# Kernel optimization log

Measured on AMD Instinct MI355X. Metric: run time of the kernel, lower is better.

The kernel has to match this reference:

```python
import jax, jax.numpy as jnp
from jax import lax
import numpy as np

S, B, XD = 2048, 64, 64   # seq_len, batch, x_dim
DX = 128                   # dense_x[-1]
H = 256                    # dim_RNN
DH = 128                   # dense_h_x[-1]
ALPHAS = np.array([0.9, 0.5, 0.1, 0.01], dtype=np.float32)


def setup_inputs() -> dict:
    key = jax.random.key(0)
    ks = jax.random.split(key, 12)
    def lin(k, fan_in, shape):
        return jax.random.normal(k, shape, jnp.float32) / np.sqrt(fan_in)
    sigmas = jnp.asarray(-np.log(1.0 / ALPHAS - 1.0), jnp.float32)  # inverse sigmoid
    return {
        "x": jax.random.normal(ks[0], (S, B, XD), jnp.float32),
        "Wx": lin(ks[1], XD, (XD, DX)),   # feature_extractor_x linear
        "bx": jnp.zeros((DX,), jnp.float32),
        "Wih": lin(ks[2], DX, (H, DX)),   # RNN input-hidden
        "bih": jnp.zeros((H,), jnp.float32),
        "Whh": lin(ks[3], H, (H, H)),     # RNN hidden-hidden
        "bhh": jnp.zeros((H,), jnp.float32),
        "Whx": lin(ks[4], H, (H, DH)),    # mlp_h_x linear
        "bhx": jnp.zeros((DH,), jnp.float32),
        "Wout": lin(ks[5], DH, (DH, XD)), # gen_out
        "bout": jnp.zeros((XD,), jnp.float32),
        "sigmas": sigmas,
    }


def reference(x, Wx, bx, Wih, bih, Whh, bhh, Whx, bhx, Wout, bout, sigmas):
    # alphas_per_unit: sigmoid(sigmas) tiled to dim_RNN
    alphas = jnp.tile(jax.nn.sigmoid(sigmas), H // sigmas.shape[0])  # [H]
    # feature extractor over all timesteps (teacher forcing, mix_ratio=0)
    feat = jnp.tanh(x @ Wx + bx)  # [S, B, DX]
    h0 = jnp.zeros((x.shape[1], H), x.dtype)

    def step(h, f_t):
        # emit y_t from previous hidden state: gen_out(tanh(mlp_h_x(h)))
        y_t = jnp.tanh(h @ Whx + bhx) @ Wout + bout        # [B, XD]
        # single-step Elman RNN cell
        h_new = jnp.tanh(f_t @ Wih.T + bih + h @ Whh.T + bhh)
        # leaky integration blend per unit
        h_next = (1.0 - alphas) * h + alphas * h_new
        return h_next, y_t

    _, y = lax.scan(step, h0, feat)  # y: [S, B, XD]
    return y
```

## Files before the change

### kernel.cpp

```cpp
#include <hip/hip_runtime.h>
#include <math.h>

#define SS 2048
#define BB 64
#define XDIM 64
#define DXF 128
#define HH 256
#define DHH 128
#define CHUNK 16
#define NW (SS / CHUNK)

typedef float v2f __attribute__((ext_vector_type(2)));

__device__ __forceinline__ float ftanh(float x) {
    float e = __expf(2.0f * x);
    return 1.0f - 2.0f / (e + 1.0f);
}

template <int CTRL>
__device__ __forceinline__ float dpp_mov_f(float x) {
    return __int_as_float(__builtin_amdgcn_update_dpp(
        0, __float_as_int(x), CTRL, 0xF, 0xF, true));
}

__global__ __launch_bounds__(256) void k1_featu(
    const float* __restrict__ x, const float* __restrict__ Wx,
    const float* __restrict__ bx, const float* __restrict__ Wih,
    const float* __restrict__ bih, const float* __restrict__ bhh,
    float* __restrict__ u)
{
    __shared__ float xs[64][XDIM];
    __shared__ float fs[64][DXF];
    const int tid = threadIdx.x;
    const size_t row0 = (size_t)blockIdx.x * 64;

    for (int v = tid; v < 64 * XDIM; v += 256) {
        int r = v >> 6, m = v & 63;
        xs[r][m] = x[(row0 + r) * XDIM + m];
    }
    __syncthreads();

    {
        const int cq = tid & 31;
        const int ru = tid >> 5;
        v2f aA[2][4], aB[2][4];
        #pragma unroll
        for (int g = 0; g < 2; ++g)
            #pragma unroll
            for (int i = 0; i < 4; ++i) { aA[g][i] = (v2f)0.f; aB[g][i] = (v2f)0.f; }

        #pragma unroll
        for (int kc = 0; kc < 4; ++kc) {
            v2f wA[16], wB[16];
            #pragma unroll
            for (int k = 0; k < 16; ++k) {
                const float* wp = Wx + (kc * 16 + k) * DXF + cq;
                wA[k] = (v2f){wp[0],  wp[32]};
                wB[k] = (v2f){wp[64], wp[96]};
            }
            #pragma unroll
            for (int g = 0; g < 2; ++g) {
                const int rb = 8 * ru + 4 * g;
                #pragma unroll
                for (int k4 = 0; k4 < 4; ++k4) {
                    float4 xv[4];
                    #pragma unroll
                    for (int i = 0; i < 4; ++i)
                        xv[i] = *(const float4*)&xs[rb + i][kc * 16 + 4 * k4];
                    #pragma unroll
                    for (int i = 0; i < 4; ++i) {
                        #pragma unroll
                        for (int e = 0; e < 4; ++e) {
                            const float xe = (e == 0) ? xv[i].x : (e == 1) ? xv[i].y
                                           : (e == 2) ? xv[i].z : xv[i].w;
                            const v2f xb = (v2f){xe, xe};
                            aA[g][i] += wA[4 * k4 + e] * xb;
                            aB[g][i] += wB[4 * k4 + e] * xb;
                        }
                    }
                }
            }
        }
        const float b0 = bx[cq], b1 = bx[cq + 32], b2 = bx[cq + 64], b3 = bx[cq + 96];
        #pragma unroll
        for (int g = 0; g < 2; ++g)
            #pragma unroll
            for (int i = 0; i < 4; ++i) {
                const int r = 8 * ru + 4 * g + i;
                fs[r][cq]      = ftanh(aA[g][i].x + b0);
                fs[r][cq + 32] = ftanh(aA[g][i].y + b1);
                fs[r][cq + 64] = ftanh(aB[g][i].x + b2);
                fs[r][cq + 96] = ftanh(aB[g][i].y + b3);
            }
    }
    __syncthreads();

    {
        const int q4 = tid & 63;
        const int rq = tid >> 6;
        v2f aA[4][4], aB[4][4];
        #pragma unroll
        for (int g = 0; g < 4; ++g)
            #pragma unroll
            for (int i = 0; i < 4; ++i) { aA[g][i] = (v2f)0.f; aB[g][i] = (v2f)0.f; }

        #pragma unroll
        for (int kc = 0; kc < 8; ++kc) {
            v2f wA[16], wB[16];
            #pragma unroll
            for (int k4 = 0; k4 < 4; ++k4) {
                const float4 w0 = *(const float4*)(Wih + (size_t)(q4      ) * DXF + kc * 16 + 4 * k4);
                const float4 w1 = *(const float4*)(Wih + (size_t)(q4 +  64) * DXF + kc * 16 + 4 * k4);
                const float4 w2 = *(const float4*)(Wih + (size_t)(q4 + 128) * DXF + kc * 16 + 4 * k4);
                const float4 w3 = *(const float4*)(Wih + (size_t)(q4 + 192) * DXF + kc * 16 + 4 * k4);
                wA[4 * k4 + 0] = (v2f){w0.x, w1.x}; wA[4 * k4 + 1] = (v2f){w0.y, w1.y};
                wA[4 * k4 + 2] = (v2f){w0.z, w1.z}; wA[4 * k4 + 3] = (v2f){w0.w, w1.w};
                wB[4 * k4 + 0] = (v2f){w2.x, w3.x}; wB[4 * k4 + 1] = (v2f){w2.y, w3.y};
                wB[4 * k4 + 2] = (v2f){w2.z, w3.z}; wB[4 * k4 + 3] = (v2f){w2.w, w3.w};
            }
            #pragma unroll
            for (int g = 0; g < 4; ++g) {
                const int rb = 16 * rq + 4 * g;
                #pragma unroll
                for (int k4 = 0; k4 < 4; ++k4) {
                    float4 fv[4];
                    #pragma unroll
                    for (int i = 0; i < 4; ++i)
                        fv[i] = *(const float4*)&fs[rb + i][kc * 16 + 4 * k4];
                    #pragma unroll
                    for (int i = 0; i < 4; ++i) {
                        #pragma unroll
                        for (int e = 0; e < 4; ++e) {
                            const float fe = (e == 0) ? fv[i].x : (e == 1) ? fv[i].y
                                           : (e == 2) ? fv[i].z : fv[i].w;
                            const v2f fb = (v2f){fe, fe};
                            aA[g][i] += wA[4 * k4 + e] * fb;
                            aB[g][i] += wB[4 * k4 + e] * fb;
                        }
                    }
                }
            }
        }
        const float b0 = bih[q4]       + bhh[q4];
        const float b1 = bih[q4 + 64]  + bhh[q4 + 64];
        const float b2 = bih[q4 + 128] + bhh[q4 + 128];
        const float b3 = bih[q4 + 192] + bhh[q4 + 192];
        #pragma unroll
        for (int g = 0; g < 4; ++g)
            #pragma unroll
            for (int i = 0; i < 4; ++i) {
                const size_t row = row0 + 16 * rq + 4 * g + i;
                u[row * HH + q4]       = aA[g][i].x + b0;
                u[row * HH + q4 + 64]  = aA[g][i].y + b1;
                u[row * HH + q4 + 128] = aB[g][i].x + b2;
                u[row * HH + q4 + 192] = aB[g][i].y + b3;
            }
    }
}

__global__ __launch_bounds__(1024)
__attribute__((amdgpu_waves_per_eu(4, 4)))
void k2_rnn(
    const float* __restrict__ u, const float* __restrict__ Whh,
    const float* __restrict__ sigmas, float* __restrict__ hist)
{
    __shared__ float hbuf[2][HH];
    __shared__ float ubuf[2][CHUNK][HH];
    const int tid = threadIdx.x;
    const int b = blockIdx.x;
    const int c  = tid & 15;
    const int rg = tid >> 4;

    v2f w2[4][8];
    #pragma unroll
    for (int r = 0; r < 4; ++r) {
        const float* wrow = Whh + (size_t)(4 * rg + r) * HH + 16 * c;
        #pragma unroll
        for (int j = 0; j < 4; ++j) {
            const float4 wv = *(const float4*)(wrow + 4 * j);
            w2[r][2 * j]     = (v2f){wv.x, wv.y};
            w2[r][2 * j + 1] = (v2f){wv.z, wv.w};
        }
    }
    #pragma unroll
    for (int r = 0; r < 4; r += 2) {
        asm volatile("" : "+v"(w2[r][0]),     "+v"(w2[r][1]),     "+v"(w2[r][2]),     "+v"(w2[r][3]),
                          "+v"(w2[r][4]),     "+v"(w2[r][5]),     "+v"(w2[r][6]),     "+v"(w2[r][7]),
                          "+v"(w2[r + 1][0]), "+v"(w2[r + 1][1]), "+v"(w2[r + 1][2]), "+v"(w2[r + 1][3]),
                          "+v"(w2[r + 1][4]), "+v"(w2[r + 1][5]), "+v"(w2[r + 1][6]), "+v"(w2[r + 1][7]));
    }

    const int pb0 = c & 1;
    const int pb3 = (c >> 3) & 1;
    const int rl = 2 * pb3 + pb0;
    const int myrow = 4 * rg + rl;
    const bool own = ((c & 6) == 0);

    const float alpha = 1.f / (1.f + __expf(-sigmas[myrow & 3]));

    const int wpos = 64 * ((myrow >> 2) & 3) + 4 * (myrow >> 4) + (myrow & 3);

    const int srow = tid >> 6;
    const int col4 = tid & 63;
    const size_t ustride = (size_t)BB * HH;

    if (tid < HH) hbuf[0][tid] = 0.0f;

    {
        const float4 v = *(const float4*)(u + ((size_t)srow * BB + b) * HH + 4 * col4);
        *(float4*)&ubuf[0][srow][4 * col4] = v;
    }

    float* hp = hist + (size_t)b * HH + myrow;
    float hreg = 0.f;

    __syncthreads();

#define K2_BODY(T, S, MBUF, DO_STAGE, NBUF)                                  \
    {                                                                        \
        const int cur = (T) & 1;                                             \
        const float uval = ubuf[MBUF][S][myrow];                             \
        float4 h4[4];                                                        \
        _Pragma("unroll")                                                    \
        for (int j = 0; j < 4; ++j)                                          \
            h4[j] = *(const float4*)&hbuf[cur][64 * j + 4 * c];              \
        v2f acc[4];                                                          \
        _Pragma("unroll")                                                    \
        for (int r = 0; r < 4; ++r) acc[r] = (v2f)0.f;                       \
        _Pragma("unroll")                                                    \
        for (int j = 0; j < 4; ++j) {                                        \
            const v2f hA = (v2f){h4[j].x, h4[j].y};                          \
            const v2f hB = (v2f){h4[j].z, h4[j].w};                          \
            _Pragma("unroll")                                                \
            for (int r = 0; r < 4; ++r) {                                    \
                acc[r] += w2[r][2 * j] * hA;                                 \
                acc[r] += w2[r][2 * j + 1] * hB;                             \
            }                                                                \
        }                                                                    \
        float s_[4];                                                         \
        _Pragma("unroll")                                                    \
        for (int r = 0; r < 4; ++r) s_[r] = acc[r].x + acc[r].y;             \
                   \
        float t1[2];                                                         \
        _Pragma("unroll")                                                    \
        for (int i = 0; i < 2; ++i) {                                        \
            const float g = pb3 ? s_[i] : s_[i + 2];                         \
            const float k = pb3 ? s_[i + 2] : s_[i];                         \
            t1[i] = k + dpp_mov_f<0x128>(g);                                 \
        }                                                                    \
                \
        float sr;                                                            \
        {                                                                    \
            const float g = pb0 ? t1[0] : t1[1];                             \
            const float k = pb0 ? t1[1] : t1[0];                             \
            sr = k + dpp_mov_f<0xB1>(g);                                     \
        }                                                                    \
                            \
        sr += dpp_mov_f<0x4E>(sr);                                           \
                           \
        sr += __int_as_float(__builtin_amdgcn_ds_swizzle(                    \
                  __float_as_int(sr), 0x101F));                              \
        {                                                                    \
            const float sin_ = sr + uval;                                    \
            const float hnew = hreg + alpha * (ftanh(sin_) - hreg);          \
            if (own) {                                                       \
                *hp = hreg;                        \
                hbuf[cur ^ 1][wpos] = hnew;                                  \
            }                                                                \
            hreg = hnew;                                                     \
        }                                                                    \
        hp += ustride;                                                       \
        if (DO_STAGE) {                                                      \
             \
             \
            *(float4*)&ubuf[NBUF][srow][4 * col4] = stv;                     \
        }                                                                    \
                   \
        asm volatile("s_waitcnt lgkmcnt(0)\n\ts_barrier" ::: "memory");      \
    }

    for (int m = 0; m < NW; ++m) {
        const int mbuf = m & 1;
        const int nbuf = mbuf ^ 1;
        const bool more = (m + 1 < NW);
        float4 stv;
        if (more) {
            const size_t t0 = (size_t)(CHUNK * (m + 1));
            stv = *(const float4*)(u + ((t0 + srow) * BB + b) * HH + 4 * col4);
        }
        #pragma unroll 4
        for (int s = 0; s < CHUNK; ++s) {
            const int t = CHUNK * m + s;
            const bool stage = (s == CHUNK - 1) && more;
            K2_BODY(t, s, mbuf, stage, nbuf)
        }
    }
#undef K2_BODY
}

__global__ __launch_bounds__(256) void k3_y(
    const float* __restrict__ hist, const float* __restrict__ Whx,
    const float* __restrict__ bhx, const float* __restrict__ Wout,
    const float* __restrict__ bout, float* __restrict__ y)
{
    __shared__ float hs[32][HH];
    __shared__ float gs[32][DHH];
    const int tid = threadIdx.x;
    const size_t row0 = (size_t)blockIdx.x * 32;

    for (int v = tid; v < 32 * HH; v += 256) {
        int r = v >> 8, i = v & 255;
        hs[r][i] = hist[(row0 + r) * HH + i];
    }
    __syncthreads();

    {
        const int aq = tid & 31;
        const int ru = tid >> 5;
        v2f aA[4], aB[4];
        #pragma unroll
        for (int i = 0; i < 4; ++i) { aA[i] = (v2f)0.f; aB[i] = (v2f)0.f; }

        #pragma unroll
        for (int kc = 0; kc < 16; ++kc) {
            v2f wA[16], wB[16];
            #pragma unroll
            for (int k = 0; k < 16; ++k) {
                const float* wp = Whx + (size_t)(kc * 16 + k) * DHH + aq;
                wA[k] = (v2f){wp[0],  wp[32]};
                wB[k] = (v2f){wp[64], wp[96]};
            }
            #pragma unroll
            for (int k4 = 0; k4 < 4; ++k4) {
                float4 hv[4];
                #pragma unroll
                for (int i = 0; i < 4; ++i)
                    hv[i] = *(const float4*)&hs[4 * ru + i][kc * 16 + 4 * k4];
                #pragma unroll
                for (int i = 0; i < 4; ++i) {
                    #pragma unroll
                    for (int e = 0; e < 4; ++e) {
                        const float he = (e == 0) ? hv[i].x : (e == 1) ? hv[i].y
                                       : (e == 2) ? hv[i].z : hv[i].w;
                        const v2f hb = (v2f){he, he};
                        aA[i] += wA[4 * k4 + e] * hb;
                        aB[i] += wB[4 * k4 + e] * hb;
                    }
                }
            }
        }
        const float b0 = bhx[aq], b1 = bhx[aq + 32], b2 = bhx[aq + 64], b3 = bhx[aq + 96];
        #pragma unroll
        for (int i = 0; i < 4; ++i) {
            const int r = 4 * ru + i;
            gs[r][aq]      = ftanh(aA[i].x + b0);
            gs[r][aq + 32] = ftanh(aA[i].y + b1);
            gs[r][aq + 64] = ftanh(aB[i].x + b2);
            gs[r][aq + 96] = ftanh(aB[i].y + b3);
        }
    }
    __syncthreads();

    {
        const int o2 = tid & 31;
        const int ru = tid >> 5;
        v2f acc[4];
        #pragma unroll
        for (int i = 0; i < 4; ++i) acc[i] = (v2f)0.f;

        #pragma unroll
        for (int kc = 0; kc < 2; ++kc) {
            v2f w[64];
            #pragma unroll
            for (int k = 0; k < 64; ++k) {
                const float* wp = Wout + (size_t)(kc * 64 + k) * XDIM + o2;
                w[k] = (v2f){wp[0], wp[32]};
            }
            #pragma unroll
            for (int k4 = 0; k4 < 16; ++k4) {
                float4 gv[4];
                #pragma unroll
                for (int i = 0; i < 4; ++i)
                    gv[i] = *(const float4*)&gs[4 * ru + i][kc * 64 + 4 * k4];
                #pragma unroll
                for (int i = 0; i < 4; ++i) {
                    #pragma unroll
                    for (int e = 0; e < 4; ++e) {
                        const float ge = (e == 0) ? gv[i].x : (e == 1) ? gv[i].y
                                       : (e == 2) ? gv[i].z : gv[i].w;
                        acc[i] += w[4 * k4 + e] * (v2f){ge, ge};
                    }
                }
            }
        }
        const float b0 = bout[o2], b1 = bout[o2 + 32];
        #pragma unroll
        for (int i = 0; i < 4; ++i) {
            const size_t row = row0 + 4 * ru + i;
            y[row * XDIM + o2]      = acc[i].x + b0;
            y[row * XDIM + o2 + 32] = acc[i].y + b1;
        }
    }
}

extern "C" void kernel_launch(void* const* d_in, const int* in_sizes, int n_in,
                              void* d_out, int out_size, void* d_ws, size_t ws_size,
                              hipStream_t stream) {
    const float* x      = (const float*)d_in[0];
    const float* Wx     = (const float*)d_in[1];
    const float* bx     = (const float*)d_in[2];
    const float* Wih    = (const float*)d_in[3];
    const float* bih    = (const float*)d_in[4];
    const float* Whh    = (const float*)d_in[5];
    const float* bhh    = (const float*)d_in[6];
    const float* Whx    = (const float*)d_in[7];
    const float* bhx    = (const float*)d_in[8];
    const float* Wout   = (const float*)d_in[9];
    const float* bout   = (const float*)d_in[10];
    const float* sigmas = (const float*)d_in[11];
    float* y = (float*)d_out;

    float* u    = (float*)d_ws;
    float* hist = u + (size_t)SS * BB * HH;

    k1_featu<<<(SS * BB) / 64, 256, 0, stream>>>(x, Wx, bx, Wih, bih, bhh, u);
    k2_rnn<<<BB, 1024, 0, stream>>>(u, Whh, sigmas, hist);
    k3_y<<<(SS * BB) / 32, 256, 0, stream>>>(hist, Whx, bhx, Wout, bout, y);
}
```

Baseline: 1.956 ms.

## Halve RNN block to 512 threads with eight Whh rows per thread

The recurrent kernel now launches 512 threads per batch element instead of 1024. Each thread holds eight rows of Whh in registers instead of four, and the cross-lane reduction gains one more DPP butterfly stage. Staging of the u chunk is split into two float4 loads per thread. The aim is to cut per-step barrier and synchronisation cost across fewer waves, at the price of more register pressure and a longer serial FMA chain per step.

Result: faster. 1.804 ms (-7.8%).

```diff
diff --git a/kernel.cpp b/kernel.cpp
--- a/kernel.cpp
+++ b/kernel.cpp
@@ -158,8 +158,7 @@
     }
 }
 
-__global__ __launch_bounds__(1024)
-__attribute__((amdgpu_waves_per_eu(4, 4)))
+__global__ __launch_bounds__(512)
 void k2_rnn(
     const float* __restrict__ u, const float* __restrict__ Whh,
     const float* __restrict__ sigmas, float* __restrict__ hist)
@@ -171,10 +170,10 @@
     const int c  = tid & 15;
     const int rg = tid >> 4;
 
-    v2f w2[4][8];
+    v2f w2[8][8];
     #pragma unroll
-    for (int r = 0; r < 4; ++r) {
-        const float* wrow = Whh + (size_t)(4 * rg + r) * HH + 16 * c;
+    for (int r = 0; r < 8; ++r) {
+        const float* wrow = Whh + (size_t)(8 * rg + r) * HH + 16 * c;
         #pragma unroll
         for (int j = 0; j < 4; ++j) {
             const float4 wv = *(const float4*)(wrow + 4 * j);
@@ -183,7 +182,7 @@
         }
     }
     #pragma unroll
-    for (int r = 0; r < 4; r += 2) {
+    for (int r = 0; r < 8; r += 2) {
         asm volatile("" : "+v"(w2[r][0]),     "+v"(w2[r][1]),     "+v"(w2[r][2]),     "+v"(w2[r][3]),
                           "+v"(w2[r][4]),     "+v"(w2[r][5]),     "+v"(w2[r][6]),     "+v"(w2[r][7]),
                           "+v"(w2[r + 1][0]), "+v"(w2[r + 1][1]), "+v"(w2[r + 1][2]), "+v"(w2[r + 1][3]),
@@ -191,24 +190,27 @@
     }
 
     const int pb0 = c & 1;
+    const int pb1 = (c >> 1) & 1;
     const int pb3 = (c >> 3) & 1;
-    const int rl = 2 * pb3 + pb0;
-    const int myrow = 4 * rg + rl;
-    const bool own = ((c & 6) == 0);
+    const int rl = 4 * pb3 + 2 * pb0 + pb1;
+    const int myrow = 8 * rg + rl;
+    const bool own = ((c & 4) == 0);
 
     const float alpha = 1.f / (1.f + __expf(-sigmas[myrow & 3]));
 
     const int wpos = 64 * ((myrow >> 2) & 3) + 4 * (myrow >> 4) + (myrow & 3);
 
-    const int srow = tid >> 6;
-    const int col4 = tid & 63;
+    const int s0 = tid >> 6,          c40 = tid & 63;
+    const int s1 = (tid + 512) >> 6,  c41 = tid & 63;
     const size_t ustride = (size_t)BB * HH;
 
     if (tid < HH) hbuf[0][tid] = 0.0f;
 
     {
-        const float4 v = *(const float4*)(u + ((size_t)srow * BB + b) * HH + 4 * col4);
-        *(float4*)&ubuf[0][srow][4 * col4] = v;
+        const float4 v0 = *(const float4*)(u + ((size_t)s0 * BB + b) * HH + 4 * c40);
+        const float4 v1 = *(const float4*)(u + ((size_t)s1 * BB + b) * HH + 4 * c41);
+        *(float4*)&ubuf[0][s0][4 * c40] = v0;
+        *(float4*)&ubuf[0][s1][4 * c41] = v1;
     }
 
     float* hp = hist + (size_t)b * HH + myrow;
@@ -224,40 +226,46 @@
         _Pragma("unroll")                                                    \
         for (int j = 0; j < 4; ++j)                                          \
             h4[j] = *(const float4*)&hbuf[cur][64 * j + 4 * c];              \
-        v2f acc[4];                                                          \
-        _Pragma("unroll")                                                    \
-        for (int r = 0; r < 4; ++r) acc[r] = (v2f)0.f;                       \
+        v2f acc[8];                                                          \
+        _Pragma("unroll")                                                    \
+        for (int r = 0; r < 8; ++r) acc[r] = (v2f)0.f;                       \
         _Pragma("unroll")                                                    \
         for (int j = 0; j < 4; ++j) {                                        \
             const v2f hA = (v2f){h4[j].x, h4[j].y};                          \
             const v2f hB = (v2f){h4[j].z, h4[j].w};                          \
             _Pragma("unroll")                                                \
-            for (int r = 0; r < 4; ++r) {                                    \
+            for (int r = 0; r < 8; ++r) {                                    \
                 acc[r] += w2[r][2 * j] * hA;                                 \
                 acc[r] += w2[r][2 * j + 1] * hB;                             \
             }                                                                \
         }                                                                    \
-        float s_[4];                                                         \
-        _Pragma("unroll")                                                    \
-        for (int r = 0; r < 4; ++r) s_[r] = acc[r].x + acc[r].y;             \
+        float s_[8];                                                         \
+        _Pragma("unroll")                                                    \
+        for (int r = 0; r < 8; ++r) s_[r] = acc[r].x + acc[r].y;             \
                    \
-        float t1[2];                                                         \
+        float t1[4];                                                         \
+        _Pragma("unroll")                                                    \
+        for (int i = 0; i < 4; ++i) {                                        \
+            const float g = pb3 ? s_[i] : s_[i + 4];                         \
+            const float k = pb3 ? s_[i + 4] : s_[i];                         \
+            t1[i] = k + dpp_mov_f<0x128>(g);                                 \
+        }                                                                    \
+                \
+        float t2[2];                                                         \
         _Pragma("unroll")                                                    \
         for (int i = 0; i < 2; ++i) {                                        \
-            const float g = pb3 ? s_[i] : s_[i + 2];                         \
-            const float k = pb3 ? s_[i + 2] : s_[i];                         \
-            t1[i] = k + dpp_mov_f<0x128>(g);                                 \
+            const float g = pb0 ? t1[i] : t1[i + 2];                         \
+            const float k = pb0 ? t1[i + 2] : t1[i];                         \
+            t2[i] = k + dpp_mov_f<0xB1>(g);                                  \
         }                                                                    \
                 \
         float sr;                                                            \
         {                                                                    \
-            const float g = pb0 ? t1[0] : t1[1];                             \
-            const float k = pb0 ? t1[1] : t1[0];                             \
-            sr = k + dpp_mov_f<0xB1>(g);                                     \
-        }                                                                    \
-                            \
-        sr += dpp_mov_f<0x4E>(sr);                                           \
-                           \
+            const float g = pb1 ? t2[0] : t2[1];                             \
+            const float k = pb1 ? t2[1] : t2[0];                             \
+            sr = k + dpp_mov_f<0x4E>(g);                                     \
+        }                                                                    \
+                 \
         sr += __int_as_float(__builtin_amdgcn_ds_swizzle(                    \
                   __float_as_int(sr), 0x101F));                              \
         {                                                                    \
@@ -273,7 +281,8 @@
         if (DO_STAGE) {                                                      \
              \
              \
-            *(float4*)&ubuf[NBUF][srow][4 * col4] = stv;                     \
+            *(float4*)&ubuf[NBUF][s0][4 * c40] = stv0;                       \
+            *(float4*)&ubuf[NBUF][s1][4 * c41] = stv1;                       \
         }                                                                    \
                    \
         asm volatile("s_waitcnt lgkmcnt(0)\n\ts_barrier" ::: "memory");      \
@@ -283,10 +292,11 @@
         const int mbuf = m & 1;
         const int nbuf = mbuf ^ 1;
         const bool more = (m + 1 < NW);
-        float4 stv;
+        float4 stv0, stv1;
         if (more) {
             const size_t t0 = (size_t)(CHUNK * (m + 1));
-            stv = *(const float4*)(u + ((t0 + srow) * BB + b) * HH + 4 * col4);
+            stv0 = *(const float4*)(u + ((t0 + s0) * BB + b) * HH + 4 * c40);
+            stv1 = *(const float4*)(u + ((t0 + s1) * BB + b) * HH + 4 * c41);
         }
         #pragma unroll 4
         for (int s = 0; s < CHUNK; ++s) {
@@ -424,6 +434,6 @@
     float* hist = u + (size_t)SS * BB * HH;
 
     k1_featu<<<(SS * BB) / 64, 256, 0, stream>>>(x, Wx, bx, Wih, bih, bhh, u);
-    k2_rnn<<<BB, 1024, 0, stream>>>(u, Whh, sigmas, hist);
+    k2_rnn<<<BB, 512, 0, stream>>>(u, Whh, sigmas, hist);
     k3_y<<<(SS * BB) / 32, 256, 0, stream>>>(hist, Whx, bhx, Wout, bout, y);
 }
```
